# Kernel optimization log

Measured on AMD Instinct MI355X. Metric: run time of the kernel, lower is better.

The kernel has to match this reference:

```python
import jax, jax.numpy as jnp
import numpy as np

B, N_DIM, K_DIM = 16384, 4096, 128


def setup_inputs() -> dict:
    key = jax.random.key(0)
    k1, k2, k3, k4 = jax.random.split(key, 4)
    x = jax.random.normal(k1, (B, N_DIM), dtype=jnp.float32)
    # nn.Linear(n_dim, 1): weight (1, n_dim), bias (1,)
    lim = 1.0 / np.sqrt(N_DIM)
    W = jax.random.uniform(k2, (1, N_DIM), dtype=jnp.float32, minval=-lim, maxval=lim)
    b = jax.random.uniform(k3, (1,), dtype=jnp.float32, minval=-lim, maxval=lim)
    # V initialized N(0, 0.001)
    V = 0.001 * jax.random.normal(k4, (N_DIM, K_DIM), dtype=jnp.float32)
    return {"x": x, "W": W, "b": b, "V": V}


def reference(x, W, b, V):
    # linear part: (B,1)
    linear = x @ W.T + b
    # term1 = 0.5 * sum_k (x @ V)_k^2  (torch code's 'sum_of_square')
    xv = x @ V  # (B, k)
    term1 = 0.5 * jnp.sum(xv * xv, axis=1, keepdims=True)
    # term2: torch's expand+matmul+bmm reduces algebraically to
    # -0.5 * (sum_i x_i)^2 * ||V.sum(0)||^2  (identical math, no (B,n,n) tensor)
    s = jnp.sum(V, axis=0)  # (k,)
    xsum = jnp.sum(x, axis=1, keepdims=True)  # (B,1)
    term2 = -0.5 * (xsum * xsum) * jnp.dot(s, s)
    return linear + term1 + term2
```

## Files before the change

### kernel.cpp

```cpp
#include <hip/hip_runtime.h>

typedef __bf16 bf16;
typedef __bf16 bf16x8 __attribute__((ext_vector_type(8)));
typedef float f32x16 __attribute__((ext_vector_type(16)));

#define B_ROWS 16384
#define N_DIM  4096
#define K_DIM  128

__global__ __launch_bounds__(256) void prep_kernel(const float* __restrict__ V,
                                                   float* __restrict__ spart,
                                                   bf16* __restrict__ Ut) {
    __shared__ bf16 tile[128 * 136];
    __shared__ float sp[256];
    const int t = threadIdx.x;
    const int jbase = blockIdx.x * 128;
    const int c  = t & 127;
    const int j0 = t >> 7;

    float sacc = 0.f;
#pragma unroll 8
    for (int i = 0; i < 64; ++i) {
        int j = j0 + 2 * i;
        float v = V[(size_t)(jbase + j) * K_DIM + c];
        sacc += v;
        tile[c * 136 + j] = (bf16)v;
    }
    sp[t] = sacc;
    __syncthreads();
    if (t < 128) spart[blockIdx.x * 128 + t] = sp[t] + sp[t + 128];

    const int col = t >> 1, half = t & 1;
#pragma unroll
    for (int i = 0; i < 4; ++i) {
        uint4 d = *(const uint4*)&tile[col * 136 + half * 64 + i * 16];
        *(uint4*)&Ut[(size_t)col * N_DIM + jbase + half * 64 + i * 16] = d;
    }
}

__global__ __launch_bounds__(256, 2) void fm_main(const float* __restrict__ x,
                                                  const float* __restrict__ W,
                                                  const float* __restrict__ bptr,
                                                  const bf16* __restrict__ Ut,
                                                  const float* __restrict__ spart,
                                                  float* __restrict__ out) {
    __shared__ bf16  xs[2][32 * 72];
    __shared__ bf16  us[2][128 * 64];
    __shared__ float redxs[256];
    __shared__ float redxw[256];
    __shared__ float rowsq[4 * 32];
    __shared__ float snred[2];

    const int t    = threadIdx.x;
    const int wave = t >> 6;
    const int lane = t & 63;
    const int l31  = lane & 31;
    const int h    = lane >> 5;
    const int r0   = blockIdx.x * 32;

    const int srow = t >> 3;
    const int scg  = t & 7;

    f32x16 acc;
#pragma unroll
    for (int i = 0; i < 16; ++i) acc[i] = 0.f;

    float xsum_acc = 0.f, xw_acc = 0.f;
    const float* xrow = x + (size_t)(r0 + srow) * N_DIM + scg * 8;
    const float* wrow = W + scg * 8;
    const bf16* ub = Ut + (size_t)(wave * 32 + (lane >> 3)) * N_DIM + (lane & 7) * 8;

#pragma unroll
    for (int j = 0; j < 4; ++j) {
        __builtin_amdgcn_global_load_lds(
            (const __attribute__((address_space(1))) void*)(ub + (size_t)j * 8 * N_DIM),
            (__attribute__((address_space(3))) void*)&us[0][(wave * 32 + j * 8) * 64],
            16, 0, 0);
    }
    float4 a0 = *(const float4*)(xrow);
    float4 a1 = *(const float4*)(xrow + 4);
    float4 w0 = *(const float4*)(wrow);
    float4 w1 = *(const float4*)(wrow + 4);
    float4 b0 = *(const float4*)(xrow + 64);
    float4 b1 = *(const float4*)(xrow + 68);
    float4 v0 = *(const float4*)(wrow + 64);
    float4 v1 = *(const float4*)(wrow + 68);

    for (int it = 0; it < 64; ++it) {
        const int bsel = it & 1;
        const int kb1 = (it < 63) ? (it + 1) * 64 : 0;
        const int kb2 = (it < 62) ? (it + 2) * 64 : 0;

        bf16x8 xb;
        xb[0] = (bf16)a0.x; xb[1] = (bf16)a0.y; xb[2] = (bf16)a0.z; xb[3] = (bf16)a0.w;
        xb[4] = (bf16)a1.x; xb[5] = (bf16)a1.y; xb[6] = (bf16)a1.z; xb[7] = (bf16)a1.w;
        *(bf16x8*)&xs[bsel][srow * 72 + scg * 8] = xb;

        asm volatile("s_waitcnt lgkmcnt(0)" ::: "memory");
        __builtin_amdgcn_s_barrier();
        __builtin_amdgcn_sched_barrier(0);

#pragma unroll
        for (int j = 0; j < 4; ++j) {
            __builtin_amdgcn_global_load_lds(
                (const __attribute__((address_space(1))) void*)(ub + (size_t)j * 8 * N_DIM + kb1),
                (__attribute__((address_space(3))) void*)&us[bsel ^ 1][(wave * 32 + j * 8) * 64],
                16, 0, 0);
        }
        __builtin_amdgcn_sched_barrier(0);

        float4 n0 = *(const float4*)(xrow + kb2);
        float4 n1 = *(const float4*)(xrow + kb2 + 4);
        float4 m0 = *(const float4*)(wrow + kb2);
        float4 m1 = *(const float4*)(wrow + kb2 + 4);

        xsum_acc += (a0.x + a0.y + a0.z + a0.w) + (a1.x + a1.y + a1.z + a1.w);
        xw_acc   += a0.x * w0.x + a0.y * w0.y + a0.z * w0.z + a0.w * w0.w
                  + a1.x * w1.x + a1.y * w1.y + a1.z * w1.z + a1.w * w1.w;

        asm volatile("s_waitcnt vmcnt(12)" ::: "memory");
        __builtin_amdgcn_sched_barrier(0);

        __builtin_amdgcn_s_setprio(1);
#pragma unroll
        for (int ks = 0; ks < 64; ks += 16) {
            bf16x8 af  = *(const bf16x8*)&xs[bsel][l31 * 72 + ks + h * 8];
            bf16x8 bfv = *(const bf16x8*)&us[bsel][(wave * 32 + l31) * 64 + ks + h * 8];
            acc = __builtin_amdgcn_mfma_f32_32x32x16_bf16(af, bfv, acc, 0, 0, 0);
        }
        __builtin_amdgcn_s_setprio(0);

        a0 = b0; a1 = b1; w0 = v0; w1 = v1;
        b0 = n0; b1 = n1; v0 = m0; v1 = m1;
    }

    redxs[t] = xsum_acc;
    redxw[t] = xw_acc;

#pragma unroll
    for (int r = 0; r < 16; ++r) {
        float s = acc[r] * acc[r];
        s += __shfl_xor(s, 1);
        s += __shfl_xor(s, 2);
        s += __shfl_xor(s, 4);
        s += __shfl_xor(s, 8);
        s += __shfl_xor(s, 16);
        if (l31 == 0) {
            int row = (r & 3) + 8 * (r >> 2) + 4 * h;
            rowsq[wave * 32 + row] = s;
        }
    }

    if (t < 128) {
        float sv = 0.f;
#pragma unroll
        for (int bb = 0; bb < 32; ++bb) sv += spart[bb * 128 + t];
        float sq = sv * sv;
#pragma unroll
        for (int m = 32; m >= 1; m >>= 1) sq += __shfl_down(sq, m, 64);
        if ((t & 63) == 0) snred[t >> 6] = sq;
    }
    __syncthreads();

    if (t < 32) {
        float xsum = 0.f, xw = 0.f;
#pragma unroll
        for (int g = 0; g < 8; ++g) { xsum += redxs[t * 8 + g]; xw += redxw[t * 8 + g]; }
        float sq = rowsq[t] + rowsq[32 + t] + rowsq[64 + t] + rowsq[96 + t];
        float snorm = snred[0] + snred[1];
        float bv = bptr[0];
        out[r0 + t] = bv + xw + 0.5f * sq - 0.5f * xsum * xsum * snorm;
    }
}

extern "C" void kernel_launch(void* const* d_in, const int* in_sizes, int n_in,
                              void* d_out, int out_size, void* d_ws, size_t ws_size,
                              hipStream_t stream) {
    const float* x  = (const float*)d_in[0];
    const float* W  = (const float*)d_in[1];
    const float* bp = (const float*)d_in[2];
    const float* V  = (const float*)d_in[3];
    float* out = (float*)d_out;

    char* ws = (char*)d_ws;
    float* spart = (float*)(ws + 1024);
    bf16*  Ut    = (bf16*)(ws + 32768);

    hipLaunchKernelGGL(prep_kernel, dim3(32), dim3(256), 0, stream, V, spart, Ut);
    hipLaunchKernelGGL(fm_main, dim3(512), dim3(256), 0, stream, x, W, bp, Ut, spart, out);
}
```

Before: 397.0 us.

## Fuse V prep into main kernel via cooperative grid sync and deepen pipeline

Merges the V transpose/bf16 conversion and column-sum prep into the main kernel. Each of 512 blocks handles 8 rows of V, then a cooperative grid sync makes Ut visible to all blocks. The main loop is unrolled by two with four x staging buffers and two explicit U buffers, with async LDS loads issued after each MFMA stage. The final reduction now sums 512 partial vectors instead of 32. This removes a kernel launch and a serial dependency but adds grid-sync cost and requires all 512 blocks to be co-resident.

Result: slower. 438.9 us (+10.6%).

```diff
diff --git a/kernel.cpp b/kernel.cpp
--- a/kernel.cpp
+++ b/kernel.cpp
@@ -1,4 +1,7 @@
 #include <hip/hip_runtime.h>
+#include <hip/hip_cooperative_groups.h>
+
+namespace cg = cooperative_groups;
 
 typedef __bf16 bf16;
 typedef __bf16 bf16x8 __attribute__((ext_vector_type(8)));
@@ -8,48 +11,22 @@
 #define N_DIM  4096
 #define K_DIM  128
 
-__global__ __launch_bounds__(256) void prep_kernel(const float* __restrict__ V,
+__global__ __launch_bounds__(256, 2) void fm_fused(const float* __restrict__ x,
+                                                   const float* __restrict__ W,
+                                                   const float* __restrict__ bptr,
+                                                   const float* __restrict__ V,
                                                    float* __restrict__ spart,
-                                                   bf16* __restrict__ Ut) {
-    __shared__ bf16 tile[128 * 136];
-    __shared__ float sp[256];
-    const int t = threadIdx.x;
-    const int jbase = blockIdx.x * 128;
-    const int c  = t & 127;
-    const int j0 = t >> 7;
-
-    float sacc = 0.f;
-#pragma unroll 8
-    for (int i = 0; i < 64; ++i) {
-        int j = j0 + 2 * i;
-        float v = V[(size_t)(jbase + j) * K_DIM + c];
-        sacc += v;
-        tile[c * 136 + j] = (bf16)v;
-    }
-    sp[t] = sacc;
-    __syncthreads();
-    if (t < 128) spart[blockIdx.x * 128 + t] = sp[t] + sp[t + 128];
-
-    const int col = t >> 1, half = t & 1;
-#pragma unroll
-    for (int i = 0; i < 4; ++i) {
-        uint4 d = *(const uint4*)&tile[col * 136 + half * 64 + i * 16];
-        *(uint4*)&Ut[(size_t)col * N_DIM + jbase + half * 64 + i * 16] = d;
-    }
-}
-
-__global__ __launch_bounds__(256, 2) void fm_main(const float* __restrict__ x,
-                                                  const float* __restrict__ W,
-                                                  const float* __restrict__ bptr,
-                                                  const bf16* __restrict__ Ut,
-                                                  const float* __restrict__ spart,
-                                                  float* __restrict__ out) {
-    __shared__ bf16  xs[2][32 * 72];
+                                                   bf16* __restrict__ Ut,
+                                                   float* __restrict__ out) {
+    __shared__ bf16  xs[4][32 * 72];
     __shared__ bf16  us[2][128 * 64];
     __shared__ float redxs[256];
     __shared__ float redxw[256];
     __shared__ float rowsq[4 * 32];
+    __shared__ float sp2[256];
     __shared__ float snred[2];
+    __shared__ float spf[8 * 128];
+    __shared__ bf16  tb[128 * 10];
 
     const int t    = threadIdx.x;
     const int wave = t >> 6;
@@ -58,6 +35,33 @@
     const int h    = lane >> 5;
     const int r0   = blockIdx.x * 32;
 
+    {
+        const int vbase = blockIdx.x * 8 * 128;
+        float4 v4 = *(const float4*)(V + vbase + t * 4);
+        const int r  = t >> 5;
+        const int c0 = (t & 31) * 4;
+        spf[r * 128 + c0 + 0] = v4.x;
+        spf[r * 128 + c0 + 1] = v4.y;
+        spf[r * 128 + c0 + 2] = v4.z;
+        spf[r * 128 + c0 + 3] = v4.w;
+        tb[(c0 + 0) * 10 + r] = (bf16)v4.x;
+        tb[(c0 + 1) * 10 + r] = (bf16)v4.y;
+        tb[(c0 + 2) * 10 + r] = (bf16)v4.z;
+        tb[(c0 + 3) * 10 + r] = (bf16)v4.w;
+        __syncthreads();
+        if (t < 128) {
+            float sv = 0.f;
+#pragma unroll
+            for (int r2 = 0; r2 < 8; ++r2) sv += spf[r2 * 128 + t];
+            spart[(size_t)blockIdx.x * 128 + t] = sv;
+            union { bf16 hv[8]; uint4 u; } pk;
+#pragma unroll
+            for (int k = 0; k < 8; ++k) pk.hv[k] = tb[t * 10 + k];
+            *(uint4*)(Ut + (size_t)t * N_DIM + blockIdx.x * 8) = pk.u;
+        }
+    }
+    cg::this_grid().sync();
+
     const int srow = t >> 3;
     const int scg  = t & 7;
 
@@ -77,6 +81,14 @@
             (__attribute__((address_space(3))) void*)&us[0][(wave * 32 + j * 8) * 64],
             16, 0, 0);
     }
+#pragma unroll
+    for (int j = 0; j < 4; ++j) {
+        __builtin_amdgcn_global_load_lds(
+            (const __attribute__((address_space(1))) void*)(ub + (size_t)j * 8 * N_DIM + 64),
+            (__attribute__((address_space(3))) void*)&us[1][(wave * 32 + j * 8) * 64],
+            16, 0, 0);
+    }
+    __builtin_amdgcn_sched_barrier(0);
     float4 a0 = *(const float4*)(xrow);
     float4 a1 = *(const float4*)(xrow + 4);
     float4 w0 = *(const float4*)(wrow);
@@ -85,55 +97,89 @@
     float4 b1 = *(const float4*)(xrow + 68);
     float4 v0 = *(const float4*)(wrow + 64);
     float4 v1 = *(const float4*)(wrow + 68);
-
-    for (int it = 0; it < 64; ++it) {
-        const int bsel = it & 1;
-        const int kb1 = (it < 63) ? (it + 1) * 64 : 0;
-        const int kb2 = (it < 62) ? (it + 2) * 64 : 0;
+    __builtin_amdgcn_sched_barrier(0);
+
+    for (int p = 0; p < 32; ++p) {
+        const int i0 = 2 * p;
+        const int s0 = i0 & 3, s1 = (i0 + 1) & 3;
+        const int kb2 = ((i0 + 2 < 64) ? (i0 + 2) : 0) * 64;
+        const int kb3 = ((i0 + 3 < 64) ? (i0 + 3) : 0) * 64;
 
         bf16x8 xb;
         xb[0] = (bf16)a0.x; xb[1] = (bf16)a0.y; xb[2] = (bf16)a0.z; xb[3] = (bf16)a0.w;
         xb[4] = (bf16)a1.x; xb[5] = (bf16)a1.y; xb[6] = (bf16)a1.z; xb[7] = (bf16)a1.w;
-        *(bf16x8*)&xs[bsel][srow * 72 + scg * 8] = xb;
+        *(bf16x8*)&xs[s0][srow * 72 + scg * 8] = xb;
+        xb[0] = (bf16)b0.x; xb[1] = (bf16)b0.y; xb[2] = (bf16)b0.z; xb[3] = (bf16)b0.w;
+        xb[4] = (bf16)b1.x; xb[5] = (bf16)b1.y; xb[6] = (bf16)b1.z; xb[7] = (bf16)b1.w;
+        *(bf16x8*)&xs[s1][srow * 72 + scg * 8] = xb;
 
         asm volatile("s_waitcnt lgkmcnt(0)" ::: "memory");
         __builtin_amdgcn_s_barrier();
-        __builtin_amdgcn_sched_barrier(0);
-
-#pragma unroll
-        for (int j = 0; j < 4; ++j) {
-            __builtin_amdgcn_global_load_lds(
-                (const __attribute__((address_space(1))) void*)(ub + (size_t)j * 8 * N_DIM + kb1),
-                (__attribute__((address_space(3))) void*)&us[bsel ^ 1][(wave * 32 + j * 8) * 64],
-                16, 0, 0);
-        }
         __builtin_amdgcn_sched_barrier(0);
 
         float4 n0 = *(const float4*)(xrow + kb2);
         float4 n1 = *(const float4*)(xrow + kb2 + 4);
         float4 m0 = *(const float4*)(wrow + kb2);
         float4 m1 = *(const float4*)(wrow + kb2 + 4);
-
-        xsum_acc += (a0.x + a0.y + a0.z + a0.w) + (a1.x + a1.y + a1.z + a1.w);
+        float4 o0 = *(const float4*)(xrow + kb3);
+        float4 o1 = *(const float4*)(xrow + kb3 + 4);
+        float4 q0 = *(const float4*)(wrow + kb3);
+        float4 q1 = *(const float4*)(wrow + kb3 + 4);
+        __builtin_amdgcn_sched_barrier(0);
+
+        xsum_acc += (a0.x + a0.y + a0.z + a0.w) + (a1.x + a1.y + a1.z + a1.w)
+                  + (b0.x + b0.y + b0.z + b0.w) + (b1.x + b1.y + b1.z + b1.w);
         xw_acc   += a0.x * w0.x + a0.y * w0.y + a0.z * w0.z + a0.w * w0.w
-                  + a1.x * w1.x + a1.y * w1.y + a1.z * w1.z + a1.w * w1.w;
+                  + a1.x * w1.x + a1.y * w1.y + a1.z * w1.z + a1.w * w1.w
+                  + b0.x * v0.x + b0.y * v0.y + b0.z * v0.z + b0.w * v0.w
+                  + b1.x * v1.x + b1.y * v1.y + b1.z * v1.z + b1.w * v1.w;
+        __builtin_amdgcn_sched_barrier(0);
 
         asm volatile("s_waitcnt vmcnt(12)" ::: "memory");
         __builtin_amdgcn_sched_barrier(0);
-
         __builtin_amdgcn_s_setprio(1);
 #pragma unroll
         for (int ks = 0; ks < 64; ks += 16) {
-            bf16x8 af  = *(const bf16x8*)&xs[bsel][l31 * 72 + ks + h * 8];
-            bf16x8 bfv = *(const bf16x8*)&us[bsel][(wave * 32 + l31) * 64 + ks + h * 8];
+            bf16x8 af  = *(const bf16x8*)&xs[s0][l31 * 72 + ks + h * 8];
+            bf16x8 bfv = *(const bf16x8*)&us[0][(wave * 32 + l31) * 64 + ks + h * 8];
             acc = __builtin_amdgcn_mfma_f32_32x32x16_bf16(af, bfv, acc, 0, 0, 0);
         }
         __builtin_amdgcn_s_setprio(0);
-
-        a0 = b0; a1 = b1; w0 = v0; w1 = v1;
-        b0 = n0; b1 = n1; v0 = m0; v1 = m1;
-    }
-
+        __builtin_amdgcn_sched_barrier(0);
+#pragma unroll
+        for (int j = 0; j < 4; ++j) {
+            __builtin_amdgcn_global_load_lds(
+                (const __attribute__((address_space(1))) void*)(ub + (size_t)j * 8 * N_DIM + kb2),
+                (__attribute__((address_space(3))) void*)&us[0][(wave * 32 + j * 8) * 64],
+                16, 0, 0);
+        }
+        __builtin_amdgcn_sched_barrier(0);
+
+        asm volatile("s_waitcnt vmcnt(12)" ::: "memory");
+        __builtin_amdgcn_sched_barrier(0);
+        __builtin_amdgcn_s_setprio(1);
+#pragma unroll
+        for (int ks = 0; ks < 64; ks += 16) {
+            bf16x8 af  = *(const bf16x8*)&xs[s1][l31 * 72 + ks + h * 8];
+            bf16x8 bfv = *(const bf16x8*)&us[1][(wave * 32 + l31) * 64 + ks + h * 8];
+            acc = __builtin_amdgcn_mfma_f32_32x32x16_bf16(af, bfv, acc, 0, 0, 0);
+        }
+        __builtin_amdgcn_s_setprio(0);
+        __builtin_amdgcn_sched_barrier(0);
+#pragma unroll
+        for (int j = 0; j < 4; ++j) {
+            __builtin_amdgcn_global_load_lds(
+                (const __attribute__((address_space(1))) void*)(ub + (size_t)j * 8 * N_DIM + kb3),
+                (__attribute__((address_space(3))) void*)&us[1][(wave * 32 + j * 8) * 64],
+                16, 0, 0);
+        }
+        __builtin_amdgcn_sched_barrier(0);
+
+        a0 = n0; a1 = n1; w0 = m0; w1 = m1;
+        b0 = o0; b1 = o1; v0 = q0; v1 = q1;
+    }
+
+    __syncthreads();
     redxs[t] = xsum_acc;
     redxw[t] = xw_acc;
 
@@ -151,11 +197,17 @@
         }
     }
 
+    {
+        const int cc = t & 127, hh = t >> 7;
+        float sv = 0.f;
+#pragma unroll 8
+        for (int i = 0; i < 256; ++i) sv += spart[(size_t)(hh * 256 + i) * 128 + cc];
+        sp2[t] = sv;
+    }
+    __syncthreads();
     if (t < 128) {
-        float sv = 0.f;
-#pragma unroll
-        for (int bb = 0; bb < 32; ++bb) sv += spart[bb * 128 + t];
-        float sq = sv * sv;
+        float s2 = sp2[t] + sp2[128 + t];
+        float sq = s2 * s2;
 #pragma unroll
         for (int m = 32; m >= 1; m >>= 1) sq += __shfl_down(sq, m, 64);
         if ((t & 63) == 0) snred[t >> 6] = sq;
@@ -184,8 +236,9 @@
 
     char* ws = (char*)d_ws;
     float* spart = (float*)(ws + 1024);
-    bf16*  Ut    = (bf16*)(ws + 32768);
-
-    hipLaunchKernelGGL(prep_kernel, dim3(32), dim3(256), 0, stream, V, spart, Ut);
-    hipLaunchKernelGGL(fm_main, dim3(512), dim3(256), 0, stream, x, W, bp, Ut, spart, out);
+    bf16*  Ut    = (bf16*)(ws + 1024 + 262144);
+
+    void* args[] = { (void*)&x, (void*)&W, (void*)&bp, (void*)&V,
+                     (void*)&spart, (void*)&Ut, (void*)&out };
+    hipLaunchCooperativeKernel((void*)fm_fused, dim3(512), dim3(256), args, 0, stream);
 }
```

## Double K-tile to 128 with XOR-swizzled LDS layout and single-stage x prefetch

Applied to the files above, without the earlier changes.

Raises the per-iteration K chunk from 64 to 128, halving the loop count and barriers. The padded LDS rows are replaced by an XOR swizzle applied both on the global-to-LDS copy and on the MFMA fragment reads, to avoid bank conflicts. The x/W register prefetch drops from two stages ahead to one stage of wider loads. The reduction scratch now aliases a shared pool after a final sync. LDS use rises to 80 KB per block, which may limit occupancy below the requested two blocks per CU.

After: 371.6 us. 1.07x faster.

```diff
diff --git a/kernel.cpp b/kernel.cpp
--- a/kernel.cpp
+++ b/kernel.cpp
@@ -44,12 +44,9 @@
                                                   const bf16* __restrict__ Ut,
                                                   const float* __restrict__ spart,
                                                   float* __restrict__ out) {
-    __shared__ bf16  xs[2][32 * 72];
-    __shared__ bf16  us[2][128 * 64];
-    __shared__ float redxs[256];
-    __shared__ float redxw[256];
-    __shared__ float rowsq[4 * 32];
-    __shared__ float snred[2];
+    __shared__ __align__(16) char pool[81920];
+    bf16* xs = (bf16*)pool;
+    bf16* us = (bf16*)(pool + 16384);
 
     const int t    = threadIdx.x;
     const int wave = t >> 6;
@@ -66,73 +63,101 @@
     for (int i = 0; i < 16; ++i) acc[i] = 0.f;
 
     float xsum_acc = 0.f, xw_acc = 0.f;
-    const float* xrow = x + (size_t)(r0 + srow) * N_DIM + scg * 8;
-    const float* wrow = W + scg * 8;
-    const bf16* ub = Ut + (size_t)(wave * 32 + (lane >> 3)) * N_DIM + (lane & 7) * 8;
-
-#pragma unroll
-    for (int j = 0; j < 4; ++j) {
-        __builtin_amdgcn_global_load_lds(
-            (const __attribute__((address_space(1))) void*)(ub + (size_t)j * 8 * N_DIM),
-            (__attribute__((address_space(3))) void*)&us[0][(wave * 32 + j * 8) * 64],
-            16, 0, 0);
-    }
+    const float* xrow = x + (size_t)(r0 + srow) * N_DIM + scg * 16;
+    const float* wrow = W + scg * 16;
+    const int dr = lane >> 4;
+    const int dc = lane & 15;
+
     float4 a0 = *(const float4*)(xrow);
     float4 a1 = *(const float4*)(xrow + 4);
+    float4 a2 = *(const float4*)(xrow + 8);
+    float4 a3 = *(const float4*)(xrow + 12);
     float4 w0 = *(const float4*)(wrow);
     float4 w1 = *(const float4*)(wrow + 4);
-    float4 b0 = *(const float4*)(xrow + 64);
-    float4 b1 = *(const float4*)(xrow + 68);
-    float4 v0 = *(const float4*)(wrow + 64);
-    float4 v1 = *(const float4*)(wrow + 68);
-
-    for (int it = 0; it < 64; ++it) {
+    float4 w2 = *(const float4*)(wrow + 8);
+    float4 w3 = *(const float4*)(wrow + 12);
+    __builtin_amdgcn_sched_barrier(0);
+#pragma unroll
+    for (int j = 0; j < 8; ++j) {
+        const int rw = j * 4 + dr;
+        const bf16* src = Ut + (size_t)(wave * 32 + rw) * N_DIM
+                             + (size_t)((dc ^ (rw & 15)) * 8);
+        __builtin_amdgcn_global_load_lds(
+            (const __attribute__((address_space(1))) void*)src,
+            (__attribute__((address_space(3))) void*)&us[(wave * 32 + j * 4) * 128],
+            16, 0, 0);
+    }
+    __builtin_amdgcn_sched_barrier(0);
+
+#pragma unroll 2
+    for (int it = 0; it < 32; ++it) {
         const int bsel = it & 1;
-        const int kb1 = (it < 63) ? (it + 1) * 64 : 0;
-        const int kb2 = (it < 62) ? (it + 2) * 64 : 0;
+        const int kb1 = ((it < 31) ? (it + 1) : 0) * 128;
 
         bf16x8 xb;
         xb[0] = (bf16)a0.x; xb[1] = (bf16)a0.y; xb[2] = (bf16)a0.z; xb[3] = (bf16)a0.w;
         xb[4] = (bf16)a1.x; xb[5] = (bf16)a1.y; xb[6] = (bf16)a1.z; xb[7] = (bf16)a1.w;
-        *(bf16x8*)&xs[bsel][srow * 72 + scg * 8] = xb;
+        *(bf16x8*)&xs[bsel * 4096 + srow * 128 + (((scg * 2) ^ (srow & 15)) * 8)] = xb;
+        xb[0] = (bf16)a2.x; xb[1] = (bf16)a2.y; xb[2] = (bf16)a2.z; xb[3] = (bf16)a2.w;
+        xb[4] = (bf16)a3.x; xb[5] = (bf16)a3.y; xb[6] = (bf16)a3.z; xb[7] = (bf16)a3.w;
+        *(bf16x8*)&xs[bsel * 4096 + srow * 128 + (((scg * 2 + 1) ^ (srow & 15)) * 8)] = xb;
 
         asm volatile("s_waitcnt lgkmcnt(0)" ::: "memory");
         __builtin_amdgcn_s_barrier();
         __builtin_amdgcn_sched_barrier(0);
 
-#pragma unroll
-        for (int j = 0; j < 4; ++j) {
+        float4 n0 = *(const float4*)(xrow + kb1);
+        float4 n1 = *(const float4*)(xrow + kb1 + 4);
+        float4 n2 = *(const float4*)(xrow + kb1 + 8);
+        float4 n3 = *(const float4*)(xrow + kb1 + 12);
+        float4 m0 = *(const float4*)(wrow + kb1);
+        float4 m1 = *(const float4*)(wrow + kb1 + 4);
+        float4 m2 = *(const float4*)(wrow + kb1 + 8);
+        float4 m3 = *(const float4*)(wrow + kb1 + 12);
+        __builtin_amdgcn_sched_barrier(0);
+
+#pragma unroll
+        for (int j = 0; j < 8; ++j) {
+            const int rw = j * 4 + dr;
+            const bf16* src = Ut + (size_t)(wave * 32 + rw) * N_DIM + kb1
+                                 + (size_t)((dc ^ (rw & 15)) * 8);
             __builtin_amdgcn_global_load_lds(
-                (const __attribute__((address_space(1))) void*)(ub + (size_t)j * 8 * N_DIM + kb1),
-                (__attribute__((address_space(3))) void*)&us[bsel ^ 1][(wave * 32 + j * 8) * 64],
+                (const __attribute__((address_space(1))) void*)src,
+                (__attribute__((address_space(3))) void*)&us[(bsel ^ 1) * 16384 + (wave * 32 + j * 4) * 128],
                 16, 0, 0);
         }
         __builtin_amdgcn_sched_barrier(0);
 
-        float4 n0 = *(const float4*)(xrow + kb2);
-        float4 n1 = *(const float4*)(xrow + kb2 + 4);
-        float4 m0 = *(const float4*)(wrow + kb2);
-        float4 m1 = *(const float4*)(wrow + kb2 + 4);
-
-        xsum_acc += (a0.x + a0.y + a0.z + a0.w) + (a1.x + a1.y + a1.z + a1.w);
+        xsum_acc += (a0.x + a0.y + a0.z + a0.w) + (a1.x + a1.y + a1.z + a1.w)
+                  + (a2.x + a2.y + a2.z + a2.w) + (a3.x + a3.y + a3.z + a3.w);
         xw_acc   += a0.x * w0.x + a0.y * w0.y + a0.z * w0.z + a0.w * w0.w
-                  + a1.x * w1.x + a1.y * w1.y + a1.z * w1.z + a1.w * w1.w;
-
-        asm volatile("s_waitcnt vmcnt(12)" ::: "memory");
+                  + a1.x * w1.x + a1.y * w1.y + a1.z * w1.z + a1.w * w1.w
+                  + a2.x * w2.x + a2.y * w2.y + a2.z * w2.z + a2.w * w2.w
+                  + a3.x * w3.x + a3.y * w3.y + a3.z * w3.z + a3.w * w3.w;
+
+        asm volatile("s_waitcnt vmcnt(16)" ::: "memory");
         __builtin_amdgcn_sched_barrier(0);
 
         __builtin_amdgcn_s_setprio(1);
 #pragma unroll
-        for (int ks = 0; ks < 64; ks += 16) {
-            bf16x8 af  = *(const bf16x8*)&xs[bsel][l31 * 72 + ks + h * 8];
-            bf16x8 bfv = *(const bf16x8*)&us[bsel][(wave * 32 + l31) * 64 + ks + h * 8];
+        for (int ks = 0; ks < 128; ks += 16) {
+            const int ch = (ks >> 3) + h;
+            const int cx = (ch ^ (l31 & 15)) * 8;
+            bf16x8 af  = *(const bf16x8*)&xs[bsel * 4096 + l31 * 128 + cx];
+            bf16x8 bfv = *(const bf16x8*)&us[bsel * 16384 + (wave * 32 + l31) * 128 + cx];
             acc = __builtin_amdgcn_mfma_f32_32x32x16_bf16(af, bfv, acc, 0, 0, 0);
         }
         __builtin_amdgcn_s_setprio(0);
 
-        a0 = b0; a1 = b1; w0 = v0; w1 = v1;
-        b0 = n0; b1 = n1; v0 = m0; v1 = m1;
-    }
+        a0 = n0; a1 = n1; a2 = n2; a3 = n3;
+        w0 = m0; w1 = m1; w2 = m2; w3 = m3;
+    }
+
+    __syncthreads();
+    float* redxs  = (float*)pool;
+    float* redxw  = redxs + 256;
+    float* rowsq  = redxw + 256;
+    float* snred  = rowsq + 128;
 
     redxs[t] = xsum_acc;
     redxw[t] = xw_acc;
```
